# Optimization experiments

Hardware: AMD Instinct MI355X
Metric: run time of the kernel (lower is better)

## Reference

```python
import jax, jax.numpy as jnp
import numpy as np
from jax import lax

N_CLASS, EMB, HID, NUM_LAYER = 32000, 256, 512, 2
BATCH, SEQ = 128, 512


def setup_inputs() -> dict:
    key = jax.random.key(0)
    ks = jax.random.split(key, 8)
    s = 0.05
    return {
        "X": jax.random.randint(ks[0], (BATCH, SEQ), 0, N_CLASS),
        "C": jax.random.normal(ks[1], (N_CLASS, EMB), jnp.float32) * s,
        "W_ax": jax.random.normal(ks[2], (HID, EMB), jnp.float32) * s,
        "W_aa": jax.random.normal(ks[3], (HID, HID), jnp.float32) * s,   # shared across all layers ([m]*n quirk)
        "W_aa_l": jax.random.normal(ks[4], (HID, HID), jnp.float32) * s, # shared inter-layer weight
        "b_a": jnp.ones((HID,), jnp.float32),                            # shared bias
        "W_out": jax.random.normal(ks[5], (N_CLASS, HID), jnp.float32) * s,
        "b_out": jnp.ones((N_CLASS,), jnp.float32),
    }


def reference(X, C, W_ax, W_aa, W_aa_l, b_a, W_out, b_out):
    emb = C[X]                       # [B, T, E]
    xs = jnp.swapaxes(emb, 0, 1)     # [T, B, E] time-major
    B = X.shape[0]

    def step(m, x):                  # m: [L, B, H]
        h0 = jnp.tanh(x @ W_ax.T + m[0] @ W_aa.T + b_a)
        hs = [h0]
        for l in range(1, NUM_LAYER):
            hs.append(jnp.tanh(hs[l - 1] @ W_aa_l.T + m[l] @ W_aa.T + b_a))
        return jnp.stack(hs), None

    m0 = jnp.zeros((NUM_LAYER, B, HID), emb.dtype)
    m_final, _ = lax.scan(step, m0, xs)
    return m_final[NUM_LAYER - 1] @ W_out.T + b_out  # [B, n_class]
```

## Files before the change

### kernel.cpp

```cpp
#include <hip/hip_runtime.h>
#include <hip/hip_bf16.h>
#include <stdint.h>


#define VOCAB 32000
#define EMB   256
#define HID   512
#define BATCH 128
#define SEQ   512
#define SLOT  8192
#define FSTRIDE 32

typedef __attribute__((ext_vector_type(8))) short bf16x8;
typedef __attribute__((ext_vector_type(4))) float f32x4;

__device__ inline short f2bf(float f) {
  union { float f; uint32_t u; } v; v.f = f;
  uint32_t u = v.u;
  uint32_t r = (u + 0x7FFFu + ((u >> 16) & 1u)) >> 16;
  return (short)r;
}
__device__ inline float bf2f(unsigned short s) {
  union { uint32_t u; float f; } v; v.u = ((uint32_t)s) << 16;
  return v.f;
}
__device__ inline bf16x8 cvt8(f32x4 x0, f32x4 x1) {
  bf16x8 r;
  r[0]=f2bf(x0[0]); r[1]=f2bf(x0[1]); r[2]=f2bf(x0[2]); r[3]=f2bf(x0[3]);
  r[4]=f2bf(x1[0]); r[5]=f2bf(x1[1]); r[6]=f2bf(x1[2]); r[7]=f2bf(x1[3]);
  return r;
}
__device__ inline f32x4 mfma16(bf16x8 a, bf16x8 b, f32x4 c) {
  return __builtin_amdgcn_mfma_f32_16x16x32_bf16(a, b, c, 0, 0, 0);
}
__device__ inline float fast_tanh(float x) {
  x = fminf(30.f, fmaxf(-30.f, x));
  float e = __expf(2.f * x);
  return (e - 1.f) * __builtin_amdgcn_rcpf(e + 1.f);
}

#define VMCNT0  asm volatile("s_waitcnt vmcnt(0)" ::: "memory")
#define VMCNT16 asm volatile("s_waitcnt vmcnt(16)" ::: "memory")
#define LGKM0   asm volatile("s_waitcnt lgkmcnt(0)" ::: "memory")
#define SCHED0  __builtin_amdgcn_sched_barrier(0)

__device__ inline void st16(unsigned short* p, bf16x8 v) {
  asm volatile("global_store_dwordx4 %0, %1, off sc0 sc1" :: "v"(p), "v"(v) : "memory");
}
__device__ inline void sig(unsigned* p, unsigned v) {
  asm volatile("global_store_dword %0, %1, off sc0 sc1" :: "v"(p), "v"(v) : "memory");
}
__device__ inline void poll2(const unsigned* f0, const unsigned* f1,
                             unsigned t0, unsigned t1) {
  const int lane = threadIdx.x & 63;
  bool ok = (lane >= 32);
  const unsigned* fp = (lane < 16) ? (f0 + lane * FSTRIDE)
                                   : (f1 + (lane - 16) * FSTRIDE);
  const unsigned tgt = (lane < 16) ? t0 : t1;
  unsigned v = 0; int guard = 0;
  while (__ballot(ok) != ~0ull) {
    if (!ok) {
      asm volatile("global_load_dword %0, %1, off sc0 sc1\n\ts_waitcnt vmcnt(0)"
                   : "=v"(v) : "v"(fp) : "memory");
      ok = (v >= tgt);
    }
    if (__ballot(ok) == ~0ull) break;
    __builtin_amdgcn_s_sleep(1);
    if (++guard > 30000) break;
  }
}

__global__ void k_init(unsigned* __restrict__ p, int n) {
  int i = blockIdx.x * 256 + threadIdx.x;
  if (i < n) p[i] = 0u;
}

__global__ void __launch_bounds__(256) k_cw(const float* __restrict__ C,
                                            const float* __restrict__ Wax,
                                            unsigned short* __restrict__ CW) {
  const int tid = threadIdx.x, lane = tid & 63, wv = tid >> 6;
  const int l15 = lane & 15, l4 = lane >> 4;
  const int row = blockIdx.x * 64 + wv * 16 + l15;
  bf16x8 a[8];
  const float* crow = C + (size_t)row * EMB;
#pragma unroll
  for (int s = 0; s < 8; ++s) {
    const f32x4* p = (const f32x4*)(crow + s * 32 + l4 * 8);
    a[s] = cvt8(p[0], p[1]);
  }
  const int row_o_base = blockIdx.x * 64 + wv * 16 + l4 * 4;
  for (int ct = 0; ct < 8; ++ct) {
    f32x4 acc[4];
#pragma unroll
    for (int nf = 0; nf < 4; ++nf) acc[nf] = (f32x4){0.f, 0.f, 0.f, 0.f};
#pragma unroll
    for (int s = 0; s < 8; ++s) {
#pragma unroll
      for (int nf = 0; nf < 4; ++nf) {
        int col = ct * 64 + nf * 16 + l15;
        const f32x4* bp = (const f32x4*)(Wax + (size_t)col * EMB + s * 32 + l4 * 8);
        bf16x8 b = cvt8(bp[0], bp[1]);
        acc[nf] = mfma16(a[s], b, acc[nf]);
      }
    }
#pragma unroll
    for (int nf = 0; nf < 4; ++nf) {
      int col = ct * 64 + nf * 16 + l15;
#pragma unroll
      for (int r = 0; r < 4; ++r)
        CW[(size_t)(row_o_base + r) * HID + col] = (unsigned short)f2bf(acc[nf][r]);
    }
  }
}

__global__ void __launch_bounds__(256, 1) k_scan(
    const int* __restrict__ X, const float* __restrict__ Waa, const float* __restrict__ Wal,
    const float* __restrict__ ba, const unsigned short* __restrict__ CW,
    unsigned short* __restrict__ h0buf, unsigned short* __restrict__ h1buf,
    unsigned* __restrict__ flags, int NS) {
  extern __shared__ unsigned short lds[];
  unsigned short* ldsWaa = lds;
  unsigned short* ldsWal = lds + 64 * 512;
  unsigned short* packb  = lds + 2 * 64 * 512;
  const int tid = threadIdx.x, lane = tid & 63, wv = tid >> 6;
  const int l15 = lane & 15, l4 = lane >> 4;
  const int g = blockIdx.x & 7, mem = blockIdx.x >> 3;
  const int colslice = mem * 64;
  const int NM = NS - 1;
  unsigned* fl = flags + g * (32 * FSTRIDE);
  unsigned* f0 = fl;
  unsigned* f1 = fl + 16 * FSTRIDE;

  for (int c = tid; c < 64 * 64; c += 256) {
    int row = c >> 6, u = c & 63, us = u ^ (row & 7);
    {
      const f32x4* p = (const f32x4*)(Waa + (size_t)(colslice + row) * HID + u * 8);
      *(bf16x8*)(ldsWaa + row * 512 + us * 8) = cvt8(p[0], p[1]);
    }
    {
      const f32x4* p = (const f32x4*)(Wal + (size_t)(colslice + row) * HID + u * 8);
      *(bf16x8*)(ldsWal + row * 512 + us * 8) = cvt8(p[0], p[1]);
    }
  }

  const int cb  = (wv & 1) * 2;
  const int jc0 = colslice + cb * 16 + l15;
  const int jc1 = jc0 + 16;
  const float ba0 = ba[jc0], ba1 = ba[jc1];
  const int wb0 = (cb * 16 + l15) * 512;
  const int wb1 = wb0 + 16 * 512;
  const int swz = l15 & 7;
  const int aoff = l4 * 128 + l15 * 8;
  unsigned short* pk = packb + wv * 512;
  const int pl0 = ((l15 >> 3) + 0) * 128 + (l4 * 4) * 8 + (l15 & 7);
  const int pl1 = ((l15 >> 3) + 2) * 128 + (l4 * 4) * 8 + (l15 & 7);
  const int stbase = mem * 1024 + cb * 256 + lane * 8;
  const int brow = g * 16 + l4 * 4;
  unsigned short* h0g = h0buf + (size_t)g * ((size_t)NS * SLOT);
  unsigned short* h1g = h1buf + (size_t)g * ((size_t)NS * SLOT);
  __syncthreads();

#define WFRAG(W, wb, s) (*(const bf16x8*)((W) + (wb) + ((((s) * 4 + l4) ^ swz) * 8)))
#define LOAD16(arr, base)                                                         \
  _Pragma("unroll") for (int s = 0; s < 16; ++s)                                  \
    asm volatile("global_load_dwordx4 %0, %1, off sc0 sc1"                        \
                 : "=v"(arr[s]) : "v"((base) + s * 1024) : "memory");

  if (wv < 2) {
    unsigned* myf = f0 + (2 * mem + (wv & 1)) * FSTRIDE;
    int idxA[4];
    unsigned cw0[4], cw1[4];
    {
      int id0[4];
#pragma unroll
      for (int r = 0; r < 4; ++r)
        asm volatile("global_load_dword %0, %1, off"
                     : "=v"(id0[r]) : "v"(X + (size_t)(brow + r) * SEQ) : "memory");
      VMCNT0; SCHED0;
#pragma unroll
      for (int r = 0; r < 4; ++r) {
        const unsigned short* c0 = CW + (size_t)id0[r] * HID + jc0;
        asm volatile("global_load_ushort %0, %1, off" : "=v"(cw0[r]) : "v"(c0) : "memory");
        asm volatile("global_load_ushort %0, %1, off" : "=v"(cw1[r]) : "v"(c0 + 16) : "memory");
      }
#pragma unroll
      for (int r = 0; r < 4; ++r)
        asm volatile("global_load_dword %0, %1, off"
                     : "=v"(idxA[r]) : "v"(X + (size_t)(brow + r) * SEQ + 1) : "memory");
    }
    const int bpk = NS - 2;
    for (int t = 0; t < SEQ; ++t) {
      poll2(f0, f1, (unsigned)t, (unsigned)(t >= bpk ? t - bpk : 0));
      bf16x8 a0[16];
      const char* pa0 = (const char*)(h0g + (size_t)((t + NM) & NM) * SLOT + aoff);
      LOAD16(a0, pa0)
      VMCNT0; SCHED0;
      f32x4 acc0 = (f32x4){0.f, 0.f, 0.f, 0.f};
      f32x4 acc1 = (f32x4){0.f, 0.f, 0.f, 0.f};
#pragma unroll
      for (int s = 0; s < 16; ++s) {
        bf16x8 a = a0[s];
        acc0 = mfma16(a, WFRAG(ldsWaa, wb0, s), acc0);
        acc1 = mfma16(a, WFRAG(ldsWaa, wb1, s), acc1);
      }
#pragma unroll
      for (int r = 0; r < 4; ++r) {
        float v0 = fast_tanh(acc0[r] + bf2f((unsigned short)cw0[r]) + ba0);
        float v1 = fast_tanh(acc1[r] + bf2f((unsigned short)cw1[r]) + ba1);
        pk[pl0 + r * 8] = (unsigned short)f2bf(v0);
        pk[pl1 + r * 8] = (unsigned short)f2bf(v1);
      }
      LGKM0; SCHED0;
      bf16x8 ov = *(const bf16x8*)(pk + lane * 8);
      st16(h0g + (size_t)(t & NM) * SLOT + stbase, ov);
      VMCNT0;
      if (lane == 0) sig(myf, (unsigned)(t + 1));
#pragma unroll
      for (int r = 0; r < 4; ++r) {
        const unsigned short* c0 = CW + (size_t)idxA[r] * HID + jc0;
        asm volatile("global_load_ushort %0, %1, off" : "=v"(cw0[r]) : "v"(c0) : "memory");
        asm volatile("global_load_ushort %0, %1, off" : "=v"(cw1[r]) : "v"(c0 + 16) : "memory");
      }
      const int tp = (t + 2 < SEQ) ? t + 2 : SEQ - 1;
#pragma unroll
      for (int r = 0; r < 4; ++r)
        asm volatile("global_load_dword %0, %1, off"
                     : "=v"(idxA[r]) : "v"(X + (size_t)(brow + r) * SEQ + tp) : "memory");
    }
  } else {
    unsigned* myf = f1 + (2 * mem + (wv & 1)) * FSTRIDE;
    for (int t = 0; t <= SEQ; ++t) {
      poll2(f0, f1, (unsigned)t, (unsigned)t);
      if (t >= 1) {
        bf16x8 a1[16], a2[16];
        const char* pa1 = (const char*)(h0g + (size_t)((t + NM) & NM) * SLOT + aoff);
        const char* pa2 = (const char*)(h1g + (size_t)((t + NM - 1) & NM) * SLOT + aoff);
        LOAD16(a1, pa1)
        LOAD16(a2, pa2)
        VMCNT16; SCHED0;
        f32x4 acc0 = (f32x4){0.f, 0.f, 0.f, 0.f};
        f32x4 acc1 = (f32x4){0.f, 0.f, 0.f, 0.f};
#pragma unroll
        for (int s = 0; s < 16; ++s) {
          bf16x8 a = a1[s];
          acc0 = mfma16(a, WFRAG(ldsWal, wb0, s), acc0);
          acc1 = mfma16(a, WFRAG(ldsWal, wb1, s), acc1);
        }
        VMCNT0; SCHED0;
#pragma unroll
        for (int s = 0; s < 16; ++s) {
          bf16x8 a = a2[s];
          acc0 = mfma16(a, WFRAG(ldsWaa, wb0, s), acc0);
          acc1 = mfma16(a, WFRAG(ldsWaa, wb1, s), acc1);
        }
#pragma unroll
        for (int r = 0; r < 4; ++r) {
          float v0 = fast_tanh(acc0[r] + ba0);
          float v1 = fast_tanh(acc1[r] + ba1);
          pk[pl0 + r * 8] = (unsigned short)f2bf(v0);
          pk[pl1 + r * 8] = (unsigned short)f2bf(v1);
        }
        LGKM0; SCHED0;
        bf16x8 ov = *(const bf16x8*)(pk + lane * 8);
        st16(h1g + (size_t)((t + NM) & NM) * SLOT + stbase, ov);
        VMCNT0;
      }
      if (lane == 0) sig(myf, (unsigned)(t + 1));
    }
  }
#undef LOAD16
#undef WFRAG
}

__global__ void __launch_bounds__(256) k_out(const float* __restrict__ Wout,
                                             const float* __restrict__ bout,
                                             const unsigned short* __restrict__ h1buf,
                                             float* __restrict__ out, int NS) {
  const int tid = threadIdx.x, lane = tid & 63, wv = tid >> 6;
  const int l15 = lane & 15, l4 = lane >> 4;
  const int col = blockIdx.x * 64 + wv * 16 + l15;
  const float bo = bout[col];
  const int finslot = (SEQ - 1) & (NS - 1);
  f32x4 acc[8];
#pragma unroll
  for (int rt = 0; rt < 8; ++rt) acc[rt] = (f32x4){0.f, 0.f, 0.f, 0.f};
  const int aoff = l4 * 128 + l15 * 8;
#pragma unroll 4
  for (int s = 0; s < 16; ++s) {
    const f32x4* bp = (const f32x4*)(Wout + (size_t)col * HID + s * 32 + l4 * 8);
    bf16x8 b = cvt8(bp[0], bp[1]);
#pragma unroll
    for (int rt = 0; rt < 8; ++rt) {
      const unsigned short* ap = h1buf + ((size_t)rt * NS + finslot) * SLOT + aoff + s * 512;
      acc[rt] = mfma16(*(const bf16x8*)ap, b, acc[rt]);
    }
  }
#pragma unroll
  for (int rt = 0; rt < 8; ++rt) {
#pragma unroll
    for (int r = 0; r < 4; ++r) {
      int row = rt * 16 + l4 * 4 + r;
      out[(size_t)row * VOCAB + col] = acc[rt][r] + bo;
    }
  }
}

extern "C" void kernel_launch(void* const* d_in, const int* in_sizes, int n_in,
                              void* d_out, int out_size, void* d_ws, size_t ws_size,
                              hipStream_t stream) {
  const int*   X    = (const int*)d_in[0];
  const float* C    = (const float*)d_in[1];
  const float* Wax  = (const float*)d_in[2];
  const float* Waa  = (const float*)d_in[3];
  const float* Wal  = (const float*)d_in[4];
  const float* ba   = (const float*)d_in[5];
  const float* Wout = (const float*)d_in[6];
  const float* bout = (const float*)d_in[7];
  float* out = (float*)d_out;
  char* ws = (char*)d_ws;
  (void)in_sizes; (void)n_in; (void)out_size;

  const size_t cw_bytes = (size_t)VOCAB * HID * 2;
  const size_t fl_bytes = 8ull * 32 * FSTRIDE * 4;
  const size_t hb8 = 8ull * 8 * SLOT * 2;
  const size_t hb4 = 8ull * 4 * SLOT * 2;
  int NS; size_t h_bytes;
  if      (ws_size >= cw_bytes + 2 * hb8 + fl_bytes) { NS = 8; h_bytes = hb8; }
  else if (ws_size >= cw_bytes + 2 * hb4 + fl_bytes) { NS = 4; h_bytes = hb4; }
  else return;

  unsigned short* CWp = (unsigned short*)(ws);
  unsigned short* h0  = (unsigned short*)(ws + cw_bytes);
  unsigned short* h1  = (unsigned short*)(ws + cw_bytes + h_bytes);
  unsigned*       fl  = (unsigned*)(ws + cw_bytes + 2 * h_bytes);

  const int zero_words = (int)((2 * h_bytes + fl_bytes) / 4);
  hipLaunchKernelGGL(k_init, dim3((zero_words + 255) / 256), dim3(256), 0, stream,
                     (unsigned*)(ws + cw_bytes), zero_words);
  hipLaunchKernelGGL(k_cw, dim3(VOCAB / 64), dim3(256), 0, stream, C, Wax, CWp);
  hipFuncSetAttribute((const void*)k_scan, hipFuncAttributeMaxDynamicSharedMemorySize, 135168);
  hipLaunchKernelGGL(k_scan, dim3(64), dim3(256), 135168, stream,
                     X, Waa, Wal, ba, CWp, h0, h1, fl, NS);
  hipLaunchKernelGGL(k_out, dim3(VOCAB / 64), dim3(256), 0, stream, Wout, bout, h1, out, NS);
}
```

Before: 1.899 ms.

## Replace flag polling with sentinel-tagged ring slots for data-driven synchronization

Consumers no longer wait on per-step flags before loading. They load the hidden-state slot directly and check it for a 0xFFFF sentinel marker, retrying until valid data is present. After each step, producers write sentinels into a slot two steps ahead, so validity travels with the data and the flag round trip plus the store-wait before signalling are removed. Layer-0 waves still poll layer-1 flags for back-pressure, but with looser slack. This depends on bf16 values never equalling 0xFFFF in the probed element and on the ordering of global stores. It also adds extra fill kernels and forces NS=8.

```diff
diff --git a/kernel.cpp b/kernel.cpp
--- a/kernel.cpp
+++ b/kernel.cpp
@@ -6,9 +6,10 @@
 #define VOCAB 32000
 #define EMB   256
 #define HID   512
-#define BATCH 128
 #define SEQ   512
 #define SLOT  8192
+#define NS    8
+#define NM    7
 #define FSTRIDE 32
 
 typedef __attribute__((ext_vector_type(8))) short bf16x8;
@@ -40,7 +41,6 @@
 }
 
 #define VMCNT0  asm volatile("s_waitcnt vmcnt(0)" ::: "memory")
-#define VMCNT16 asm volatile("s_waitcnt vmcnt(16)" ::: "memory")
 #define LGKM0   asm volatile("s_waitcnt lgkmcnt(0)" ::: "memory")
 #define SCHED0  __builtin_amdgcn_sched_barrier(0)
 
@@ -50,29 +50,35 @@
 __device__ inline void sig(unsigned* p, unsigned v) {
   asm volatile("global_store_dword %0, %1, off sc0 sc1" :: "v"(p), "v"(v) : "memory");
 }
-__device__ inline void poll2(const unsigned* f0, const unsigned* f1,
-                             unsigned t0, unsigned t1) {
-  const int lane = threadIdx.x & 63;
-  bool ok = (lane >= 32);
-  const unsigned* fp = (lane < 16) ? (f0 + lane * FSTRIDE)
-                                   : (f1 + (lane - 16) * FSTRIDE);
-  const unsigned tgt = (lane < 16) ? t0 : t1;
-  unsigned v = 0; int guard = 0;
-  while (__ballot(ok) != ~0ull) {
-    if (!ok) {
-      asm volatile("global_load_dword %0, %1, off sc0 sc1\n\ts_waitcnt vmcnt(0)"
-                   : "=v"(v) : "v"(fp) : "memory");
-      ok = (v >= tgt);
-    }
-    if (__ballot(ok) == ~0ull) break;
-    __builtin_amdgcn_s_sleep(1);
-    if (++guard > 30000) break;
-  }
-}
-
-__global__ void k_init(unsigned* __restrict__ p, int n) {
+#define LOAD16(arr, base)                                                         \
+  _Pragma("unroll") for (int s = 0; s < 16; ++s)                                  \
+    asm volatile("global_load_dwordx4 %0, %1, off sc0 sc1"                        \
+                 : "=v"(arr[s]) : "v"((base) + s * 1024) : "memory");
+__device__ inline unsigned sbad(const bf16x8* a) {
+  unsigned bad = 0;
+#pragma unroll
+  for (int s = 0; s < 16; ++s) bad |= ((unsigned short)a[s][1] == 0xFFFFu);
+  return bad;
+}
+
+__global__ void k_fill(unsigned* __restrict__ p, int n, unsigned val) {
   int i = blockIdx.x * 256 + threadIdx.x;
-  if (i < n) p[i] = 0u;
+  if (i < n) p[i] = val;
+}
+__global__ void k_zslots(unsigned* __restrict__ h0, unsigned* __restrict__ h1,
+                         unsigned* __restrict__ fl) {
+  int i = blockIdx.x * 256 + threadIdx.x;
+  const int perT = 8 * (SLOT / 2);
+  if (i < perT) {
+    int g = i / (SLOT / 2), o = i % (SLOT / 2);
+    h0[(size_t)(g * NS + NM) * (SLOT / 2) + o] = 0u;
+  } else if (i < 2 * perT) {
+    int j = i - perT;
+    int g = j / (SLOT / 2), o = j % (SLOT / 2);
+    h1[(size_t)(g * NS + NM) * (SLOT / 2) + o] = 0u;
+  } else if (i < 2 * perT + 8 * 32 * FSTRIDE) {
+    fl[i - 2 * perT] = 0u;
+  }
 }
 
 __global__ void __launch_bounds__(256) k_cw(const float* __restrict__ C,
@@ -117,7 +123,7 @@
     const int* __restrict__ X, const float* __restrict__ Waa, const float* __restrict__ Wal,
     const float* __restrict__ ba, const unsigned short* __restrict__ CW,
     unsigned short* __restrict__ h0buf, unsigned short* __restrict__ h1buf,
-    unsigned* __restrict__ flags, int NS) {
+    unsigned* __restrict__ flags) {
   extern __shared__ unsigned short lds[];
   unsigned short* ldsWaa = lds;
   unsigned short* ldsWal = lds + 64 * 512;
@@ -126,10 +132,7 @@
   const int l15 = lane & 15, l4 = lane >> 4;
   const int g = blockIdx.x & 7, mem = blockIdx.x >> 3;
   const int colslice = mem * 64;
-  const int NM = NS - 1;
-  unsigned* fl = flags + g * (32 * FSTRIDE);
-  unsigned* f0 = fl;
-  unsigned* f1 = fl + 16 * FSTRIDE;
+  unsigned* f1 = flags + g * (32 * FSTRIDE) + 16 * FSTRIDE;
 
   for (int c = tid; c < 64 * 64; c += 256) {
     int row = c >> 6, u = c & 63, us = u ^ (row & 7);
@@ -158,16 +161,14 @@
   const int brow = g * 16 + l4 * 4;
   unsigned short* h0g = h0buf + (size_t)g * ((size_t)NS * SLOT);
   unsigned short* h1g = h1buf + (size_t)g * ((size_t)NS * SLOT);
+  bf16x8 SENT;
+#pragma unroll
+  for (int i = 0; i < 8; ++i) SENT[i] = (short)0xFFFF;
   __syncthreads();
 
 #define WFRAG(W, wb, s) (*(const bf16x8*)((W) + (wb) + ((((s) * 4 + l4) ^ swz) * 8)))
-#define LOAD16(arr, base)                                                         \
-  _Pragma("unroll") for (int s = 0; s < 16; ++s)                                  \
-    asm volatile("global_load_dwordx4 %0, %1, off sc0 sc1"                        \
-                 : "=v"(arr[s]) : "v"((base) + s * 1024) : "memory");
 
   if (wv < 2) {
-    unsigned* myf = f0 + (2 * mem + (wv & 1)) * FSTRIDE;
     int idxA[4];
     unsigned cw0[4], cw1[4];
     {
@@ -188,13 +189,26 @@
         asm volatile("global_load_dword %0, %1, off"
                      : "=v"(idxA[r]) : "v"(X + (size_t)(brow + r) * SEQ + 1) : "memory");
     }
-    const int bpk = NS - 2;
+    const unsigned* myfl = f1 + l15 * FSTRIDE;
     for (int t = 0; t < SEQ; ++t) {
-      poll2(f0, f1, (unsigned)t, (unsigned)(t >= bpk ? t - bpk : 0));
       bf16x8 a0[16];
       const char* pa0 = (const char*)(h0g + (size_t)((t + NM) & NM) * SLOT + aoff);
-      LOAD16(a0, pa0)
-      VMCNT0; SCHED0;
+      const unsigned ftgt = (t >= 5) ? (unsigned)(t - 5) : 0u;
+      {
+        int gd = 0;
+        while (true) {
+          unsigned fv = 0;
+          LOAD16(a0, pa0)
+          if (lane < 16)
+            asm volatile("global_load_dword %0, %1, off sc0 sc1"
+                         : "=v"(fv) : "v"(myfl) : "memory");
+          VMCNT0; SCHED0;
+          bool ok = (sbad(a0) == 0u) && ((lane >= 16) || (fv >= ftgt));
+          if (__ballot(ok) == ~0ull) break;
+          __builtin_amdgcn_s_sleep(1);
+          if (++gd > 30000) break;
+        }
+      }
       f32x4 acc0 = (f32x4){0.f, 0.f, 0.f, 0.f};
       f32x4 acc1 = (f32x4){0.f, 0.f, 0.f, 0.f};
 #pragma unroll
@@ -213,8 +227,8 @@
       LGKM0; SCHED0;
       bf16x8 ov = *(const bf16x8*)(pk + lane * 8);
       st16(h0g + (size_t)(t & NM) * SLOT + stbase, ov);
-      VMCNT0;
-      if (lane == 0) sig(myf, (unsigned)(t + 1));
+      if (t < SEQ - 2)
+        st16(h0g + (size_t)((t + 2) & NM) * SLOT + stbase, SENT);
 #pragma unroll
       for (int r = 0; r < 4; ++r) {
         const unsigned short* c0 = CW + (size_t)idxA[r] * HID + jc0;
@@ -227,60 +241,67 @@
         asm volatile("global_load_dword %0, %1, off"
                      : "=v"(idxA[r]) : "v"(X + (size_t)(brow + r) * SEQ + tp) : "memory");
     }
+    VMCNT0;
   } else {
     unsigned* myf = f1 + (2 * mem + (wv & 1)) * FSTRIDE;
-    for (int t = 0; t <= SEQ; ++t) {
-      poll2(f0, f1, (unsigned)t, (unsigned)t);
-      if (t >= 1) {
-        bf16x8 a1[16], a2[16];
-        const char* pa1 = (const char*)(h0g + (size_t)((t + NM) & NM) * SLOT + aoff);
-        const char* pa2 = (const char*)(h1g + (size_t)((t + NM - 1) & NM) * SLOT + aoff);
-        LOAD16(a1, pa1)
-        LOAD16(a2, pa2)
-        VMCNT16; SCHED0;
-        f32x4 acc0 = (f32x4){0.f, 0.f, 0.f, 0.f};
-        f32x4 acc1 = (f32x4){0.f, 0.f, 0.f, 0.f};
-#pragma unroll
-        for (int s = 0; s < 16; ++s) {
-          bf16x8 a = a1[s];
-          acc0 = mfma16(a, WFRAG(ldsWal, wb0, s), acc0);
-          acc1 = mfma16(a, WFRAG(ldsWal, wb1, s), acc1);
+    for (int t = 1; t <= SEQ; ++t) {
+      bf16x8 a1[16], a2[16];
+      const char* pa1 = (const char*)(h0g + (size_t)((t + NM) & NM) * SLOT + aoff);
+      const char* pa2 = (const char*)(h1g + (size_t)((t + NM - 1) & NM) * SLOT + aoff);
+      {
+        int gd = 0;
+        while (true) {
+          LOAD16(a1, pa1)
+          LOAD16(a2, pa2)
+          VMCNT0; SCHED0;
+          bool ok = ((sbad(a1) | sbad(a2)) == 0u);
+          if (__ballot(ok) == ~0ull) break;
+          __builtin_amdgcn_s_sleep(1);
+          if (++gd > 30000) break;
         }
-        VMCNT0; SCHED0;
-#pragma unroll
-        for (int s = 0; s < 16; ++s) {
-          bf16x8 a = a2[s];
-          acc0 = mfma16(a, WFRAG(ldsWaa, wb0, s), acc0);
-          acc1 = mfma16(a, WFRAG(ldsWaa, wb1, s), acc1);
-        }
-#pragma unroll
-        for (int r = 0; r < 4; ++r) {
-          float v0 = fast_tanh(acc0[r] + ba0);
-          float v1 = fast_tanh(acc1[r] + ba1);
-          pk[pl0 + r * 8] = (unsigned short)f2bf(v0);
-          pk[pl1 + r * 8] = (unsigned short)f2bf(v1);
-        }
-        LGKM0; SCHED0;
-        bf16x8 ov = *(const bf16x8*)(pk + lane * 8);
-        st16(h1g + (size_t)((t + NM) & NM) * SLOT + stbase, ov);
-        VMCNT0;
-      }
-      if (lane == 0) sig(myf, (unsigned)(t + 1));
-    }
-  }
-#undef LOAD16
+      }
+      if (lane == 0) sig(myf, (unsigned)t);
+      f32x4 acc0 = (f32x4){0.f, 0.f, 0.f, 0.f};
+      f32x4 acc1 = (f32x4){0.f, 0.f, 0.f, 0.f};
+#pragma unroll
+      for (int s = 0; s < 16; ++s) {
+        bf16x8 a = a1[s];
+        acc0 = mfma16(a, WFRAG(ldsWal, wb0, s), acc0);
+        acc1 = mfma16(a, WFRAG(ldsWal, wb1, s), acc1);
+      }
+#pragma unroll
+      for (int s = 0; s < 16; ++s) {
+        bf16x8 a = a2[s];
+        acc0 = mfma16(a, WFRAG(ldsWaa, wb0, s), acc0);
+        acc1 = mfma16(a, WFRAG(ldsWaa, wb1, s), acc1);
+      }
+#pragma unroll
+      for (int r = 0; r < 4; ++r) {
+        float v0 = fast_tanh(acc0[r] + ba0);
+        float v1 = fast_tanh(acc1[r] + ba1);
+        pk[pl0 + r * 8] = (unsigned short)f2bf(v0);
+        pk[pl1 + r * 8] = (unsigned short)f2bf(v1);
+      }
+      LGKM0; SCHED0;
+      bf16x8 ov = *(const bf16x8*)(pk + lane * 8);
+      st16(h1g + (size_t)((t + NM) & NM) * SLOT + stbase, ov);
+      if (t <= SEQ - 2)
+        st16(h1g + (size_t)((t + 1) & NM) * SLOT + stbase, SENT);
+    }
+    VMCNT0;
+  }
 #undef WFRAG
 }
 
 __global__ void __launch_bounds__(256) k_out(const float* __restrict__ Wout,
                                              const float* __restrict__ bout,
                                              const unsigned short* __restrict__ h1buf,
-                                             float* __restrict__ out, int NS) {
+                                             float* __restrict__ out) {
   const int tid = threadIdx.x, lane = tid & 63, wv = tid >> 6;
   const int l15 = lane & 15, l4 = lane >> 4;
   const int col = blockIdx.x * 64 + wv * 16 + l15;
   const float bo = bout[col];
-  const int finslot = (SEQ - 1) & (NS - 1);
+  const int finslot = (SEQ - 1) & NM;
   f32x4 acc[8];
 #pragma unroll
   for (int rt = 0; rt < 8; ++rt) acc[rt] = (f32x4){0.f, 0.f, 0.f, 0.f};
@@ -321,25 +342,26 @@
   (void)in_sizes; (void)n_in; (void)out_size;
 
   const size_t cw_bytes = (size_t)VOCAB * HID * 2;
+  const size_t hb = 8ull * NS * SLOT * 2;
   const size_t fl_bytes = 8ull * 32 * FSTRIDE * 4;
-  const size_t hb8 = 8ull * 8 * SLOT * 2;
-  const size_t hb4 = 8ull * 4 * SLOT * 2;
-  int NS; size_t h_bytes;
-  if      (ws_size >= cw_bytes + 2 * hb8 + fl_bytes) { NS = 8; h_bytes = hb8; }
-  else if (ws_size >= cw_bytes + 2 * hb4 + fl_bytes) { NS = 4; h_bytes = hb4; }
-  else return;
+  if (ws_size < cw_bytes + 2 * hb + fl_bytes) return;
 
   unsigned short* CWp = (unsigned short*)(ws);
   unsigned short* h0  = (unsigned short*)(ws + cw_bytes);
-  unsigned short* h1  = (unsigned short*)(ws + cw_bytes + h_bytes);
-  unsigned*       fl  = (unsigned*)(ws + cw_bytes + 2 * h_bytes);
-
-  const int zero_words = (int)((2 * h_bytes + fl_bytes) / 4);
-  hipLaunchKernelGGL(k_init, dim3((zero_words + 255) / 256), dim3(256), 0, stream,
-                     (unsigned*)(ws + cw_bytes), zero_words);
+  unsigned short* h1  = (unsigned short*)(ws + cw_bytes + hb);
+  unsigned*       fl  = (unsigned*)(ws + cw_bytes + 2 * hb);
+
+  const int ring_words = (int)(hb / 4);
+  hipLaunchKernelGGL(k_fill, dim3((ring_words + 255) / 256), dim3(256), 0, stream,
+                     (unsigned*)h0, ring_words, 0xFFFFFFFFu);
+  hipLaunchKernelGGL(k_fill, dim3((ring_words + 255) / 256), dim3(256), 0, stream,
+                     (unsigned*)h1, ring_words, 0xFFFFFFFFu);
+  const int zn = 2 * 8 * (SLOT / 2) + 8 * 32 * FSTRIDE;
+  hipLaunchKernelGGL(k_zslots, dim3((zn + 255) / 256), dim3(256), 0, stream,
+                     (unsigned*)h0, (unsigned*)h1, fl);
   hipLaunchKernelGGL(k_cw, dim3(VOCAB / 64), dim3(256), 0, stream, C, Wax, CWp);
   hipFuncSetAttribute((const void*)k_scan, hipFuncAttributeMaxDynamicSharedMemorySize, 135168);
   hipLaunchKernelGGL(k_scan, dim3(64), dim3(256), 135168, stream,
-                     X, Waa, Wal, ba, CWp, h0, h1, fl, NS);
-  hipLaunchKernelGGL(k_out, dim3(VOCAB / 64), dim3(256), 0, stream, Wout, bout, h1, out, NS);
-}
+                     X, Waa, Wal, ba, CWp, h0, h1, fl);
+  hipLaunchKernelGGL(k_out, dim3(VOCAB / 64), dim3(256), 0, stream, Wout, bout, h1, out);
+}
```

Result: no change. 1.869 ms (-1.6%).
